# Performance work log

Measured on AMD Instinct MI355X. Metric: run time of the kernel, lower is better.

Reference implementation:

```python
import jax, jax.numpy as jnp
import numpy as np

B, H, S, D = 4, 16, 2048, 128

def setup_inputs() -> dict:
    key = jax.random.key(0)
    kk, kq, kv = jax.random.split(key, 3)
    k = jax.random.normal(kk, (B, H, S, D), dtype=jnp.float32)
    q = jax.random.normal(kq, (B, H, S, D), dtype=jnp.float32)
    v = jax.random.normal(kv, (B, H, S, D), dtype=jnp.float32)
    # causal mask: True = masked out (strictly upper triangle)
    mask = jnp.triu(jnp.ones((S, S), dtype=bool), k=1)
    return {"k": k, "q": q, "v": v, "mask": mask}

def reference(k, q, v, mask):
    d_k = k.shape[-1]
    # scores: [B, H, S, S]
    scores = jnp.einsum("bhqd,bhkd->bhqk", q, k) / jnp.sqrt(jnp.asarray(d_k, q.dtype))
    scores = jnp.where(mask, -jnp.inf, scores)
    # numerically stable softmax over last dim (matches manual max/exp/sum)
    p = jax.nn.softmax(scores, axis=-1)
    return jnp.einsum("bhqk,bhkd->bhqd", p, v)
```

## Files before the change

### kernel.cpp

```cpp
#include <hip/hip_runtime.h>
#include <hip/hip_bf16.h>
#include <math.h>

#define BATCH 4
#define HEADS 16
#define SEQ   2048
#define DIM   128
#define BHN   (BATCH*HEADS)

#define BQ 128
#define WQ 32
#define KT 32
#define NXB (SEQ/BQ)

typedef short bf16x8 __attribute__((ext_vector_type(8)));
typedef float f32x4  __attribute__((ext_vector_type(4)));

static __device__ __forceinline__ unsigned short f2bf(float f) {
    union { float f; unsigned u; } x; x.f = f;
    unsigned r = x.u + 0x7FFF + ((x.u >> 16) & 1);
    return (unsigned short)(r >> 16);
}

static __device__ __forceinline__ void async_cp16(const unsigned short* g, unsigned short* l) {
    __builtin_amdgcn_global_load_lds(
        (const __attribute__((address_space(1))) unsigned int*)g,
        (__attribute__((address_space(3))) unsigned int*)l,
        16, 0, 0);
}

__global__ __launch_bounds__(256) void cvt_kv(
    const float* __restrict__ k, const float* __restrict__ v,
    unsigned short* __restrict__ kb, unsigned short* __restrict__ vt) {
    __shared__ unsigned short T[DIM][72];
    const int bh = blockIdx.y;
    const int s0 = blockIdx.x * 64;
    const int t  = threadIdx.x;
    const long rbase = ((long)bh * SEQ + s0) * DIM;

    #pragma unroll
    for (int u = 0; u < 2; ++u) {
        long e = rbase + (long)(t + u * 256) * 16;
        const float* src = k + e;
        unsigned short* dst = kb + e;
        #pragma unroll
        for (int h = 0; h < 2; ++h) {
            float4 a0 = *(const float4*)(src + h * 8);
            float4 a1 = *(const float4*)(src + h * 8 + 4);
            union { uint4 u4; unsigned short s[8]; } p;
            p.s[0]=f2bf(a0.x); p.s[1]=f2bf(a0.y); p.s[2]=f2bf(a0.z); p.s[3]=f2bf(a0.w);
            p.s[4]=f2bf(a1.x); p.s[5]=f2bf(a1.y); p.s[6]=f2bf(a1.z); p.s[7]=f2bf(a1.w);
            *(uint4*)(dst + h * 8) = p.u4;
        }
    }
    {
        const int r = t >> 2, i = t & 3;
        const float* src = v + rbase + (long)r * DIM + i * 32;
        #pragma unroll
        for (int j = 0; j < 8; ++j) {
            float4 x = *(const float4*)(src + j * 4);
            const int d = i * 32 + j * 4;
            T[d + 0][r] = f2bf(x.x); T[d + 1][r] = f2bf(x.y);
            T[d + 2][r] = f2bf(x.z); T[d + 3][r] = f2bf(x.w);
        }
    }
    __syncthreads();
    {
        const int d = t >> 1, h = t & 1;
        unsigned short* dst = vt + ((long)bh * DIM + d) * SEQ + s0 + h * 32;
        #pragma unroll
        for (int m = 0; m < 4; ++m)
            *(uint4*)(dst + m * 8) = *(const uint4*)&T[d][h * 32 + m * 8];
    }
}

__global__ __launch_bounds__(256, 2) void attn_fwd(
    const float* __restrict__ qg,
    const unsigned short* __restrict__ kb,
    const unsigned short* __restrict__ vtg,
    float* __restrict__ out) {

    __shared__ unsigned short Kt[2][KT][DIM];
    __shared__ unsigned short Vt[2][DIM][KT];
    __shared__ unsigned short Pl[4][2][16][KT + 8];

    const int tid  = threadIdx.x;
    const int w    = tid >> 6;
    const int lane = tid & 63;
    const int quad = lane >> 4;
    const int ql   = lane & 15;

    const int flat = blockIdx.x;
    const int xcd  = flat & 7;
    const int slot = flat >> 3;
    const int bh   = (xcd << 3) | (slot & 7);
    const int shi  = slot >> 3;
    const int xb   = (shi < 4) ? (15 - shi)
                   : (shi < 8) ? (shi - 4)
                   : (shi < 12) ? shi
                   : (19 - shi);
    const int qb0 = xb * BQ;
    const int qw0 = qb0 + w * WQ;

    const long base = (long)bh * SEQ * DIM;
    const float scale = 0.08838834764831845f * 1.4426950408889634f;

    bf16x8 qf[2][4];
    #pragma unroll
    for (int mb = 0; mb < 2; ++mb) {
        const float* qr = qg + base + (long)(qw0 + mb * 16 + ql) * DIM;
        #pragma unroll
        for (int c = 0; c < 4; ++c) {
            const float* p = qr + c * 32 + quad * 8;
            float4 x = *(const float4*)(p);
            float4 y = *(const float4*)(p + 4);
            union { bf16x8 v; unsigned short s[8]; } u;
            u.s[0]=f2bf(x.x*scale); u.s[1]=f2bf(x.y*scale);
            u.s[2]=f2bf(x.z*scale); u.s[3]=f2bf(x.w*scale);
            u.s[4]=f2bf(y.x*scale); u.s[5]=f2bf(y.y*scale);
            u.s[6]=f2bf(y.z*scale); u.s[7]=f2bf(y.w*scale);
            qf[mb][c] = u.v;
        }
    }

    f32x4 acc[2][8];
    #pragma unroll
    for (int mb = 0; mb < 2; ++mb)
        #pragma unroll
        for (int n = 0; n < 8; ++n)
            acc[mb][n] = (f32x4){0.f, 0.f, 0.f, 0.f};

    float m_[2] = {-INFINITY, -INFINITY};
    float l_[2] = {0.f, 0.f};

    auto stage = [&](int buf, int k0) {
        #pragma unroll
        for (int i = 0; i < 2; ++i) {
            const int idx = tid + i * 256;
            const int r   = idx >> 4;
            const int chg = (idx & 15) ^ (r & 15);
            async_cp16(kb + base + (long)(k0 + r) * DIM + chg * 8,
                       &Kt[buf][0][0] + ((tid >> 6) * 64 + i * 256) * 8);
            const int d   = idx >> 2;
            const int cvg = (idx & 3) ^ ((d >> 1) & 3);
            async_cp16(vtg + base + (long)d * SEQ + k0 + cvg * 8,
                       &Vt[buf][0][0] + ((tid >> 6) * 64 + i * 256) * 8);
        }
    };

    const int ntile = (qb0 + BQ) / KT;

    stage(0, 0);

    for (int t = 0; t < ntile; ++t) {
        const int buf = t & 1;
        const int k0  = t * KT;
        __syncthreads();

        if (t + 1 < ntile) stage(buf ^ 1, k0 + KT);

        const bool active = (k0 < qw0 + WQ);
        if (active) {
            f32x4 sacc[2][2];
            #pragma unroll
            for (int mb = 0; mb < 2; ++mb)
                #pragma unroll
                for (int kk = 0; kk < 2; ++kk)
                    sacc[mb][kk] = (f32x4){0.f, 0.f, 0.f, 0.f};
            #pragma unroll
            for (int c = 0; c < 4; ++c) {
                const int sw = ((c * 4 + quad) ^ ql) * 8;
                bf16x8 kf0 = *(const bf16x8*)&Kt[buf][ql]     [sw];
                bf16x8 kf1 = *(const bf16x8*)&Kt[buf][16 + ql][sw];
                #pragma unroll
                for (int mb = 0; mb < 2; ++mb) {
                    sacc[mb][0] = __builtin_amdgcn_mfma_f32_16x16x32_bf16(kf0, qf[mb][c], sacc[mb][0], 0, 0, 0);
                    sacc[mb][1] = __builtin_amdgcn_mfma_f32_16x16x32_bf16(kf1, qf[mb][c], sacc[mb][1], 0, 0, 0);
                }
            }

            bf16x8 vf[8];
            #pragma unroll
            for (int n = 0; n < 8; ++n)
                vf[n] = *(const bf16x8*)&Vt[buf][n * 16 + ql][(quad ^ ((ql >> 1) & 3)) * 8];

            float alpha_[2];
            bool  resc_[2];
            #pragma unroll
            for (int mb = 0; mb < 2; ++mb) {
                const int qrow   = qw0 + mb * 16 + ql;
                const bool needm = (k0 + KT - 1 > qw0 + mb * 16);
                float s[2][4];
                float tmax = -INFINITY;
                #pragma unroll
                for (int kk = 0; kk < 2; ++kk)
                    #pragma unroll
                    for (int r = 0; r < 4; ++r) {
                        float sv = sacc[mb][kk][r];
                        if (needm) {
                            int kg = k0 + kk * 16 + quad * 4 + r;
                            sv = (kg <= qrow) ? sv : -INFINITY;
                        }
                        s[kk][r] = sv;
                        tmax = fmaxf(tmax, sv);
                    }
                tmax = fmaxf(tmax, __shfl_xor(tmax, 16));
                tmax = fmaxf(tmax, __shfl_xor(tmax, 32));

                const bool skip = __all(tmax <= m_[mb] + 8.0f);
                const float mnew = skip ? m_[mb] : fmaxf(m_[mb], tmax);

                float rsum = 0.f;
                #pragma unroll
                for (int kk = 0; kk < 2; ++kk) {
                    float p0 = __builtin_amdgcn_exp2f(s[kk][0] - mnew);
                    float p1 = __builtin_amdgcn_exp2f(s[kk][1] - mnew);
                    float p2 = __builtin_amdgcn_exp2f(s[kk][2] - mnew);
                    float p3 = __builtin_amdgcn_exp2f(s[kk][3] - mnew);
                    rsum += (p0 + p1) + (p2 + p3);
                    union { uint2 u; __hip_bfloat162 h[2]; } pu;
                    pu.h[0] = __float22bfloat162_rn(float2{p0, p1});
                    pu.h[1] = __float22bfloat162_rn(float2{p2, p3});
                    *(uint2*)&Pl[w][mb][ql][kk * 16 + quad * 4] = pu.u;
                }
                rsum += __shfl_xor(rsum, 16);
                rsum += __shfl_xor(rsum, 32);

                if (skip) {
                    l_[mb] += rsum;
                    alpha_[mb] = 1.f; resc_[mb] = false;
                } else {
                    const float al = __builtin_amdgcn_exp2f(m_[mb] - mnew);
                    l_[mb] = l_[mb] * al + rsum;
                    m_[mb] = mnew;
                    alpha_[mb] = al; resc_[mb] = true;
                }
            }

            bf16x8 pf0 = *(const bf16x8*)&Pl[w][0][ql][quad * 8];
            bf16x8 pf1 = *(const bf16x8*)&Pl[w][1][ql][quad * 8];

            #pragma unroll
            for (int mb = 0; mb < 2; ++mb) {
                if (resc_[mb]) {
                    #pragma unroll
                    for (int r = 0; r < 4; ++r) {
                        float ar = __shfl(alpha_[mb], quad * 4 + r);
                        #pragma unroll
                        for (int n = 0; n < 8; ++n) acc[mb][n][r] *= ar;
                    }
                }
                const bf16x8 pf = mb ? pf1 : pf0;
                #pragma unroll
                for (int n = 0; n < 8; ++n)
                    acc[mb][n] = __builtin_amdgcn_mfma_f32_16x16x32_bf16(pf, vf[n], acc[mb][n], 0, 0, 0);
            }
        }
    }

    #pragma unroll
    for (int mb = 0; mb < 2; ++mb) {
        #pragma unroll
        for (int r = 0; r < 4; ++r) {
            float lr = __shfl(l_[mb], quad * 4 + r);
            float il = 1.0f / lr;
            long orow = base + (long)(qw0 + mb * 16 + quad * 4 + r) * DIM;
            #pragma unroll
            for (int n = 0; n < 8; ++n)
                out[orow + n * 16 + ql] = acc[mb][n][r] * il;
        }
    }
}

extern "C" void kernel_launch(void* const* d_in, const int* in_sizes, int n_in,
                              void* d_out, int out_size, void* d_ws, size_t ws_size,
                              hipStream_t stream) {
    const float* k = (const float*)d_in[0];
    const float* q = (const float*)d_in[1];
    const float* v = (const float*)d_in[2];
    float* o = (float*)d_out;

    unsigned short* kb = (unsigned short*)d_ws;
    unsigned short* vt = kb + (size_t)BHN * SEQ * DIM;

    cvt_kv<<<dim3(SEQ / 64, BHN), dim3(256), 0, stream>>>(k, v, kb, vt);

    attn_fwd<<<dim3(NXB * BHN), dim3(256), 0, stream>>>(q, kb, vt, o);
}
```

Before: 352.4 us.

## Stage K/V tiles in pairs per barrier, precompute addresses, raise MFMA priority

The K/V pipeline now loads two 32-key tiles per stage into a doubled shared buffer, so each __syncthreads covers two tiles of compute instead of one. Global source pointers are computed once and advanced incrementally. s_setprio is raised around the MFMA sections to favour matrix issue across waves. The lazy-rescale threshold drops from 8 to 4. Shared memory per block doubles for K/V, which may limit occupancy, and the threshold change alters numerical headroom.

```diff
diff --git a/kernel.cpp b/kernel.cpp
--- a/kernel.cpp
+++ b/kernel.cpp
@@ -80,8 +80,8 @@
     const unsigned short* __restrict__ vtg,
     float* __restrict__ out) {
 
-    __shared__ unsigned short Kt[2][KT][DIM];
-    __shared__ unsigned short Vt[2][DIM][KT];
+    __shared__ unsigned short Kt[2][2][KT][DIM];
+    __shared__ unsigned short Vt[2][2][DIM][KT];
     __shared__ unsigned short Pl[4][2][16][KT + 8];
 
     const int tid  = threadIdx.x;
@@ -133,56 +133,71 @@
     float m_[2] = {-INFINITY, -INFINITY};
     float l_[2] = {0.f, 0.f};
 
-    auto stage = [&](int buf, int k0) {
+    const unsigned short* kap[2];
+    const unsigned short* vap[2];
+    #pragma unroll
+    for (int i = 0; i < 2; ++i) {
+        const int idx = tid + i * 256;
+        const int r   = idx >> 4;
+        const int chg = (idx & 15) ^ (r & 15);
+        kap[i] = kb + base + (long)r * DIM + chg * 8;
+        const int d   = idx >> 2;
+        const int cvg = (idx & 3) ^ ((d >> 1) & 3);
+        vap[i] = vtg + base + (long)d * SEQ + cvg * 8;
+    }
+    const int ldso = ((tid >> 6) * 64) * 8;
+
+    auto stage = [&](int pb, int ti) {
         #pragma unroll
         for (int i = 0; i < 2; ++i) {
-            const int idx = tid + i * 256;
-            const int r   = idx >> 4;
-            const int chg = (idx & 15) ^ (r & 15);
-            async_cp16(kb + base + (long)(k0 + r) * DIM + chg * 8,
-                       &Kt[buf][0][0] + ((tid >> 6) * 64 + i * 256) * 8);
-            const int d   = idx >> 2;
-            const int cvg = (idx & 3) ^ ((d >> 1) & 3);
-            async_cp16(vtg + base + (long)d * SEQ + k0 + cvg * 8,
-                       &Vt[buf][0][0] + ((tid >> 6) * 64 + i * 256) * 8);
+            async_cp16(kap[i], &Kt[pb][ti][0][0] + ldso + i * 2048);
+            async_cp16(vap[i], &Vt[pb][ti][0][0] + ldso + i * 2048);
+            kap[i] += KT * DIM;
+            vap[i] += KT;
         }
     };
 
     const int ntile = (qb0 + BQ) / KT;
-
-    stage(0, 0);
-
-    for (int t = 0; t < ntile; ++t) {
-        const int buf = t & 1;
-        const int k0  = t * KT;
+    const int npair = ntile >> 1;
+
+    stage(0, 0); stage(0, 1);
+
+    for (int p = 0; p < npair; ++p) {
+        const int pb = p & 1;
         __syncthreads();
 
-        if (t + 1 < ntile) stage(buf ^ 1, k0 + KT);
-
-        const bool active = (k0 < qw0 + WQ);
-        if (active) {
+        if (p + 1 < npair) { stage(pb ^ 1, 0); stage(pb ^ 1, 1); }
+
+        #pragma unroll
+        for (int ti = 0; ti < 2; ++ti) {
+            const int k0 = (2 * p + ti) * KT;
+            const bool active = (k0 < qw0 + WQ);
+            if (!active) continue;
+
             f32x4 sacc[2][2];
             #pragma unroll
             for (int mb = 0; mb < 2; ++mb)
                 #pragma unroll
                 for (int kk = 0; kk < 2; ++kk)
                     sacc[mb][kk] = (f32x4){0.f, 0.f, 0.f, 0.f};
+            __builtin_amdgcn_s_setprio(1);
             #pragma unroll
             for (int c = 0; c < 4; ++c) {
                 const int sw = ((c * 4 + quad) ^ ql) * 8;
-                bf16x8 kf0 = *(const bf16x8*)&Kt[buf][ql]     [sw];
-                bf16x8 kf1 = *(const bf16x8*)&Kt[buf][16 + ql][sw];
+                bf16x8 kf0 = *(const bf16x8*)&Kt[pb][ti][ql]     [sw];
+                bf16x8 kf1 = *(const bf16x8*)&Kt[pb][ti][16 + ql][sw];
                 #pragma unroll
                 for (int mb = 0; mb < 2; ++mb) {
                     sacc[mb][0] = __builtin_amdgcn_mfma_f32_16x16x32_bf16(kf0, qf[mb][c], sacc[mb][0], 0, 0, 0);
                     sacc[mb][1] = __builtin_amdgcn_mfma_f32_16x16x32_bf16(kf1, qf[mb][c], sacc[mb][1], 0, 0, 0);
                 }
             }
+            __builtin_amdgcn_s_setprio(0);
 
             bf16x8 vf[8];
             #pragma unroll
             for (int n = 0; n < 8; ++n)
-                vf[n] = *(const bf16x8*)&Vt[buf][n * 16 + ql][(quad ^ ((ql >> 1) & 3)) * 8];
+                vf[n] = *(const bf16x8*)&Vt[pb][ti][n * 16 + ql][(quad ^ ((ql >> 1) & 3)) * 8];
 
             float alpha_[2];
             bool  resc_[2];
@@ -207,7 +222,7 @@
                 tmax = fmaxf(tmax, __shfl_xor(tmax, 16));
                 tmax = fmaxf(tmax, __shfl_xor(tmax, 32));
 
-                const bool skip = __all(tmax <= m_[mb] + 8.0f);
+                const bool skip = __all(tmax <= m_[mb] + 4.0f);
                 const float mnew = skip ? m_[mb] : fmaxf(m_[mb], tmax);
 
                 float rsum = 0.f;
@@ -251,9 +266,11 @@
                     }
                 }
                 const bf16x8 pf = mb ? pf1 : pf0;
+                __builtin_amdgcn_s_setprio(1);
                 #pragma unroll
                 for (int n = 0; n < 8; ++n)
                     acc[mb][n] = __builtin_amdgcn_mfma_f32_16x16x32_bf16(pf, vf[n], acc[mb][n], 0, 0, 0);
+                __builtin_amdgcn_s_setprio(0);
             }
         }
     }
```

Measured after the change: 345.5 us. No clear change (-2.0%).
